# Kernel tuning notes

Measured on AMD Instinct MI355X. Metric: run time of the kernel, lower is better.

The kernel has to match this reference:

```python
import jax, jax.numpy as jnp
import numpy as np

B, P = 4, 50000
D_IN, COND = 3, 48
# layer l: in IN_DIMS[l] -> out OUT_DIMS[l]; dims=[3,256*8,257], skip at layer index 4
IN_DIMS  = [D_IN + COND, 256, 256, 256, 256, 256, 256, 256, 256]
OUT_DIMS = [256, 256, 256, 253, 256, 256, 256, 256, 257]
N_LIN = 9
INV_SQRT2 = np.float32(1.0 / np.sqrt(2.0))


def softplus_beta100(x):
    return jax.nn.softplus(100.0 * x) * 0.01


def setup_inputs() -> dict:
    key = jax.random.key(0)
    ks = jax.random.split(key, 2 + 2 * N_LIN)
    inp = {
        "input": jax.random.normal(ks[0], (B, P, D_IN), dtype=jnp.float32),
        "cond_pose": jax.random.normal(ks[1], (B, COND), dtype=jnp.float32),
    }
    for l in range(N_LIN):
        scale = np.float32(np.sqrt(2.0 / OUT_DIMS[l]))  # geometry-style init scale
        inp[f"W{l}"] = jax.random.normal(ks[2 + 2 * l], (OUT_DIMS[l], IN_DIMS[l]), dtype=jnp.float32) * scale
        inp[f"b{l}"] = jnp.zeros((OUT_DIMS[l],), dtype=jnp.float32)
    return inp


def reference(input, cond_pose,
              W0, b0, W1, b1, W2, b2, W3, b3, W4, b4, W5, b5, W6, b6, W7, b7, W8, b8):
    Ws = [W0, W1, W2, W3, W4, W5, W6, W7, W8]
    bs = [b0, b1, b2, b3, b4, b5, b6, b7, b8]
    nb, npnt, nd = input.shape
    x_in = input.reshape(nb * npnt, nd)                                   # (N, 3)
    c = jnp.broadcast_to(cond_pose[:, None, :], (nb, npnt, COND)).reshape(nb * npnt, COND)
    x = jnp.concatenate([x_in, c], axis=-1)                               # cond concat at layer 0
    for l in range(N_LIN):
        if l == 4:  # skip connection: concat raw input, scaled by 1/sqrt(2)
            x = jnp.concatenate([x, x_in], axis=-1) * INV_SQRT2
        x = x @ Ws[l].T + bs[l]
        if l < N_LIN - 1:
            x = softplus_beta100(x)
    return x.reshape(nb, npnt, -1)                                        # (B, P, 257)
```

## Files before the change

### kernel.cpp

```cpp
#include <hip/hip_runtime.h>


typedef __attribute__((ext_vector_type(8))) short bf16x8;
typedef __attribute__((ext_vector_type(4))) float f32x4;
typedef __attribute__((ext_vector_type(2))) float f32x2;

#define PPTS 50000

__device__ __forceinline__ short f2bf(float f) {
    union { float f; unsigned u; } v; v.f = f;
    unsigned r = v.u + 0x7fffu + ((v.u >> 16) & 1u);
    return (short)(r >> 16);
}

__device__ __forceinline__ unsigned cvt_pk_bf16(float lo, float hi) {
    unsigned r;
    asm("v_cvt_pk_bf16_f32 %0, %1, %2" : "=v"(r) : "v"(lo), "v"(hi));
    return r;
}

__device__ __forceinline__ f32x2 sp100_pair(f32x2 y) {
    const f32x2 A2 = {6.9314718e-3f, 6.9314718e-3f};
    const f32x2 B2 = {-3.11522e-3f, -3.11522e-3f};
    const f32x2 C2 = {9.8829e-4f,  9.8829e-4f};
    const f32x2 K2 = {-144.26950408889634f, -144.26950408889634f};
    const f32x2 Z2 = {0.0f, 0.0f};
    f32x2 m = __builtin_elementwise_abs(y) * K2;
    f32x2 e = {__builtin_amdgcn_exp2f(m.x), __builtin_amdgcn_exp2f(m.y)};
    f32x2 t = __builtin_elementwise_fma(C2, e, B2);
    t = __builtin_elementwise_fma(t, e, A2);
    return __builtin_elementwise_fma(e, t, __builtin_elementwise_max(y, Z2));
}

__device__ __forceinline__ int xswz(int row) {
    return (((row & 7) ^ (5 * ((row >> 3) & 1))) << 4);
}
__device__ __forceinline__ short* xaddr(short* base, int row, int col) {
    int off = ((row << 9) + (col << 1)) ^ xswz(row);
    return (short*)((char*)base + off);
}
__device__ __forceinline__ const short* xaddrc(const short* base, int row, int col) {
    int off = ((row << 9) + (col << 1)) ^ xswz(row);
    return (const short*)((const char*)base + off);
}

__global__ void prep_kernel(
    const float* __restrict__ W0, const float* __restrict__ W1, const float* __restrict__ W2,
    const float* __restrict__ W3, const float* __restrict__ W4, const float* __restrict__ W5,
    const float* __restrict__ W6, const float* __restrict__ W7, const float* __restrict__ W8,
    short* __restrict__ wbf)
{
    const int gid = blockIdx.x * blockDim.x + threadIdx.x;
    if (gid >= 68096) return;
    int l, cid; const float* Wsrc;
    if      (gid <  2048) { l = 0; cid = gid;         Wsrc = W0; }
    else if (gid < 10240) { l = 1; cid = gid -  2048; Wsrc = W1; }
    else if (gid < 18432) { l = 2; cid = gid - 10240; Wsrc = W2; }
    else if (gid < 26624) { l = 3; cid = gid - 18432; Wsrc = W3; }
    else if (gid < 34816) { l = 4; cid = gid - 26624; Wsrc = W4; }
    else if (gid < 43008) { l = 5; cid = gid - 34816; Wsrc = W5; }
    else if (gid < 51200) { l = 6; cid = gid - 43008; Wsrc = W6; }
    else if (gid < 59392) { l = 7; cid = gid - 51200; Wsrc = W7; }
    else                  { l = 8; cid = gid - 59392; Wsrc = W8; }
    const int NR   = (l == 3) ? 253 : ((l == 8) ? 257 : 256);
    const int KR   = (l == 0) ? 51 : 256;
    const int klog = (l == 0) ? 1 : 3;
    const float sc = (l == 4) ? 0.70710678f : 1.0f;
    const int lane  = cid & 63;
    const int tile  = cid >> 6;
    const int ntile = tile >> klog;
    const int ktile = tile & ((1 << klog) - 1);
    const int n  = ntile * 16 + (lane & 15);
    const int k0 = ktile * 32 + ((lane >> 4) << 3);
    bf16x8 v;
#pragma unroll
    for (int j = 0; j < 8; ++j) {
        int k = k0 + j;
        float f = (n < NR && k < KR) ? Wsrc[n * KR + k] * sc : 0.0f;
        v[j] = f2bf(f);
    }
    ((bf16x8*)wbf)[gid] = v;
}

template<int KSTEPS, int MODE>
__device__ __forceinline__ void layer_fwd(short* xb,
    const bf16x8* __restrict__ wl, const float* __restrict__ bias, int lane, int wid)
{
    const int prow = lane & 15;
    const int kg   = (lane >> 4) << 3;
    const int rb4  = (lane >> 4) << 2;
    f32x4 acc[4][4];
#pragma unroll
    for (int nii = 0; nii < 4; ++nii) {
        const int cb = (wid * 4 + nii) * 16 + rb4;
        f32x4 bv;
        if (MODE == 1 && cb == 252) { f32x4 tb = {bias[252], 0.f, 0.f, 0.f}; bv = tb; }
        else bv = *(const f32x4*)(bias + cb);
#pragma unroll
        for (int mi = 0; mi < 4; ++mi)
            acc[mi][nii] = bv;
    }
#pragma unroll 2
    for (int ks = 0; ks < KSTEPS; ++ks) {
        bf16x8 a[4], b[4];
#pragma unroll
        for (int nii = 0; nii < 4; ++nii)
            a[nii] = wl[((wid * 4 + nii) * KSTEPS + ks) * 64 + lane];
#pragma unroll
        for (int mi = 0; mi < 4; ++mi)
            b[mi] = *(const bf16x8*)xaddrc(xb, mi * 16 + prow, ks * 32 + kg);
#pragma unroll
        for (int mi = 0; mi < 4; ++mi)
#pragma unroll
            for (int nii = 0; nii < 4; ++nii)
                acc[mi][nii] = __builtin_amdgcn_mfma_f32_16x16x32_bf16(
                    a[nii], b[mi], acc[mi][nii], 0, 0, 0);
    }
#pragma unroll
    for (int nii = 0; nii < 4; ++nii)
#pragma unroll
        for (int mi = 0; mi < 4; ++mi) {
            f32x2 y0 = {acc[mi][nii][0], acc[mi][nii][1]};
            f32x2 y1 = {acc[mi][nii][2], acc[mi][nii][3]};
            f32x2 r0 = sp100_pair(y0);
            f32x2 r1 = sp100_pair(y1);
            acc[mi][nii][0] = r0.x; acc[mi][nii][1] = r0.y;
            acc[mi][nii][2] = r1.x; acc[mi][nii][3] = r1.y;
        }
    __syncthreads();
#pragma unroll
    for (int nii = 0; nii < 4; ++nii) {
        const int cb = (wid * 4 + nii) * 16 + rb4;
#pragma unroll
        for (int mi = 0; mi < 4; ++mi) {
            unsigned p01 = cvt_pk_bf16(acc[mi][nii][0], acc[mi][nii][1]);
            unsigned p23 = cvt_pk_bf16(acc[mi][nii][2], acc[mi][nii][3]);
            if (MODE == 1 && cb == 252) {
                *xaddr(xb, mi * 16 + prow, 252) = (short)(p01 & 0xffff);
            } else {
                uint2 pk; pk.x = p01; pk.y = p23;
                *(uint2*)xaddr(xb, mi * 16 + prow, cb) = pk;
            }
        }
    }
}

__global__ __launch_bounds__(256, 4) void net_kernel(
    const float* __restrict__ xin, const float* __restrict__ cond,
    const bf16x8* __restrict__ W,
    const float* __restrict__ b0, const float* __restrict__ b1, const float* __restrict__ b2,
    const float* __restrict__ b3, const float* __restrict__ b4, const float* __restrict__ b5,
    const float* __restrict__ b6, const float* __restrict__ b7, const float* __restrict__ b8,
    float* __restrict__ out)
{
    __shared__ short xb[64 * 256];
    const int t    = threadIdx.x;
    const int pt0  = blockIdx.x * 64;
    const int lane = t & 63;
    const int wid  = t >> 6;

    float sk[3] = {0.f, 0.f, 0.f};
    if (t < 64) {
#pragma unroll
        for (int c = 0; c < 3; ++c)
            sk[c] = xin[(pt0 + t) * 3 + c];
    }

    {
        const int row   = t >> 2;
        const int c0    = (t & 3) << 4;
        const int point = pt0 + row;
        const int batch = point / PPTS;
        const float* xp = xin + point * 3;
        const float* cp = cond + batch * 48;
#pragma unroll
        for (int h = 0; h < 2; ++h) {
            bf16x8 v;
#pragma unroll
            for (int i = 0; i < 8; ++i) {
                int c = c0 + h * 8 + i;
                float f = (c < 3) ? xp[c] : ((c < 51) ? cp[c - 3] : 0.0f);
                v[i] = f2bf(f);
            }
            *(bf16x8*)xaddr(xb, row, c0 + h * 8) = v;
        }
    }
    __syncthreads();

    layer_fwd<2, 0>(xb, W +     0, b0, lane, wid); __syncthreads();
    layer_fwd<8, 0>(xb, W +  2048, b1, lane, wid); __syncthreads();
    layer_fwd<8, 0>(xb, W + 10240, b2, lane, wid); __syncthreads();
    layer_fwd<8, 1>(xb, W + 18432, b3, lane, wid);
    if (t < 64) {
#pragma unroll
        for (int c = 0; c < 3; ++c)
            *xaddr(xb, t, 253 + c) = f2bf(sk[c]);
    }
    __syncthreads();
    layer_fwd<8, 0>(xb, W + 26624, b4, lane, wid); __syncthreads();
    layer_fwd<8, 0>(xb, W + 34816, b5, lane, wid); __syncthreads();
    layer_fwd<8, 0>(xb, W + 43008, b6, lane, wid); __syncthreads();
    layer_fwd<8, 0>(xb, W + 51200, b7, lane, wid); __syncthreads();

    {
        const bf16x8* wl = W + 59392;
        const int prow = lane & 15;
        const int kg   = (lane >> 4) << 3;
        const int rb4  = (lane >> 4) << 2;
        const float blast = b8[256];
#pragma unroll
        for (int half = 0; half < 2; ++half) {
            f32x4 acc[2][4];
            f32x4 acc2[2];
#pragma unroll
            for (int nii = 0; nii < 4; ++nii) {
                const int cb = (wid * 4 + nii) * 16 + rb4;
                const f32x4 bv = *(const f32x4*)(b8 + cb);
#pragma unroll
                for (int m2 = 0; m2 < 2; ++m2)
                    acc[m2][nii] = bv;
            }
            {
                f32x4 bz = {(rb4 == 0) ? blast : 0.f, 0.f, 0.f, 0.f};
                acc2[0] = bz; acc2[1] = bz;
            }
#pragma unroll 2
            for (int ks = 0; ks < 8; ++ks) {
                bf16x8 a[4], b[2], a2;
#pragma unroll
                for (int nii = 0; nii < 4; ++nii)
                    a[nii] = wl[((wid * 4 + nii) * 8 + ks) * 64 + lane];
                if (wid == 0) a2 = wl[(128 + ks) * 64 + lane];
#pragma unroll
                for (int m2 = 0; m2 < 2; ++m2)
                    b[m2] = *(const bf16x8*)xaddrc(xb, (half * 2 + m2) * 16 + prow,
                                                   ks * 32 + kg);
#pragma unroll
                for (int m2 = 0; m2 < 2; ++m2)
#pragma unroll
                    for (int nii = 0; nii < 4; ++nii)
                        acc[m2][nii] = __builtin_amdgcn_mfma_f32_16x16x32_bf16(
                            a[nii], b[m2], acc[m2][nii], 0, 0, 0);
                if (wid == 0) {
#pragma unroll
                    for (int m2 = 0; m2 < 2; ++m2)
                        acc2[m2] = __builtin_amdgcn_mfma_f32_16x16x32_bf16(
                            a2, b[m2], acc2[m2], 0, 0, 0);
                }
            }
#pragma unroll
            for (int nii = 0; nii < 4; ++nii) {
                const int cb = (wid * 4 + nii) * 16 + rb4;
#pragma unroll
                for (int m2 = 0; m2 < 2; ++m2) {
                    const int rowoff = (pt0 + (half * 2 + m2) * 16 + prow) * 257 + cb;
#pragma unroll
                    for (int r = 0; r < 4; ++r)
                        out[rowoff + r] = acc[m2][nii][r];
                }
            }
            if (wid == 0 && rb4 == 0) {
#pragma unroll
                for (int m2 = 0; m2 < 2; ++m2)
                    out[(pt0 + (half * 2 + m2) * 16 + prow) * 257 + 256]
                        = acc2[m2][0];
            }
        }
    }
}

extern "C" void kernel_launch(void* const* d_in, const int* in_sizes, int n_in,
                              void* d_out, int out_size, void* d_ws, size_t ws_size,
                              hipStream_t stream)
{
    const float* xin  = (const float*)d_in[0];
    const float* cond = (const float*)d_in[1];
    const float* Wp[9]; const float* bp[9];
    for (int l = 0; l < 9; ++l) { Wp[l] = (const float*)d_in[2 + 2 * l]; bp[l] = (const float*)d_in[3 + 2 * l]; }
    short* wbf = (short*)d_ws;

    prep_kernel<<<dim3(266), dim3(256), 0, stream>>>(
        Wp[0], Wp[1], Wp[2], Wp[3], Wp[4], Wp[5], Wp[6], Wp[7], Wp[8], wbf);
    net_kernel<<<dim3(3125), dim3(256), 0, stream>>>(
        xin, cond, (const bf16x8*)wbf,
        bp[0], bp[1], bp[2], bp[3], bp[4], bp[5], bp[6], bp[7], bp[8],
        (float*)d_out);
}
```

Baseline: 319.1 us.

## Prefetch next layer's first weight fragments during softplus epilogue and use lightweight barriers

Each layer now issues the global loads for the next layer's first k-step weight fragments before running the softplus epilogue, so the latency of the first weight load at each layer start is hidden. Block barriers become a custom sequence that waits only on LDS counters, letting outstanding global prefetches stay in flight across the barrier. Launch bounds drop from 4 to 3 blocks per SM to give room for the extra live registers, at the cost of lower occupancy.

```diff
diff --git a/kernel.cpp b/kernel.cpp
--- a/kernel.cpp
+++ b/kernel.cpp
@@ -17,6 +17,12 @@
     unsigned r;
     asm("v_cvt_pk_bf16_f32 %0, %1, %2" : "=v"(r) : "v"(lo), "v"(hi));
     return r;
+}
+
+__device__ __forceinline__ void bar_lgkm() {
+    asm volatile("s_waitcnt lgkmcnt(0)" ::: "memory");
+    __builtin_amdgcn_s_barrier();
+    __builtin_amdgcn_sched_barrier(0);
 }
 
 __device__ __forceinline__ f32x2 sp100_pair(f32x2 y) {
@@ -84,7 +90,8 @@
 
 template<int KSTEPS, int MODE>
 __device__ __forceinline__ void layer_fwd(short* xb,
-    const bf16x8* __restrict__ wl, const float* __restrict__ bias, int lane, int wid)
+    const bf16x8* __restrict__ wl, const bf16x8* __restrict__ wlnext,
+    const float* __restrict__ bias, int lane, int wid, bf16x8 (&apre)[4])
 {
     const int prow = lane & 15;
     const int kg   = (lane >> 4) << 3;
@@ -105,7 +112,8 @@
         bf16x8 a[4], b[4];
 #pragma unroll
         for (int nii = 0; nii < 4; ++nii)
-            a[nii] = wl[((wid * 4 + nii) * KSTEPS + ks) * 64 + lane];
+            a[nii] = (ks == 0) ? apre[nii]
+                               : wl[((wid * 4 + nii) * KSTEPS + ks) * 64 + lane];
 #pragma unroll
         for (int mi = 0; mi < 4; ++mi)
             b[mi] = *(const bf16x8*)xaddrc(xb, mi * 16 + prow, ks * 32 + kg);
@@ -116,6 +124,9 @@
                 acc[mi][nii] = __builtin_amdgcn_mfma_f32_16x16x32_bf16(
                     a[nii], b[mi], acc[mi][nii], 0, 0, 0);
     }
+#pragma unroll
+    for (int nii = 0; nii < 4; ++nii)
+        apre[nii] = wlnext[(wid * 4 + nii) * 512 + lane];
 #pragma unroll
     for (int nii = 0; nii < 4; ++nii)
 #pragma unroll
@@ -127,7 +138,7 @@
             acc[mi][nii][0] = r0.x; acc[mi][nii][1] = r0.y;
             acc[mi][nii][2] = r1.x; acc[mi][nii][3] = r1.y;
         }
-    __syncthreads();
+    bar_lgkm();
 #pragma unroll
     for (int nii = 0; nii < 4; ++nii) {
         const int cb = (wid * 4 + nii) * 16 + rb4;
@@ -145,7 +156,7 @@
     }
 }
 
-__global__ __launch_bounds__(256, 4) void net_kernel(
+__global__ __launch_bounds__(256, 3) void net_kernel(
     const float* __restrict__ xin, const float* __restrict__ cond,
     const bf16x8* __restrict__ W,
     const float* __restrict__ b0, const float* __restrict__ b1, const float* __restrict__ b2,
@@ -159,6 +170,11 @@
     const int lane = t & 63;
     const int wid  = t >> 6;
 
+    bf16x8 apre[4];
+#pragma unroll
+    for (int nii = 0; nii < 4; ++nii)
+        apre[nii] = W[(wid * 4 + nii) * 128 + lane];
+
     float sk[3] = {0.f, 0.f, 0.f};
     if (t < 64) {
 #pragma unroll
@@ -185,22 +201,22 @@
             *(bf16x8*)xaddr(xb, row, c0 + h * 8) = v;
         }
     }
-    __syncthreads();
-
-    layer_fwd<2, 0>(xb, W +     0, b0, lane, wid); __syncthreads();
-    layer_fwd<8, 0>(xb, W +  2048, b1, lane, wid); __syncthreads();
-    layer_fwd<8, 0>(xb, W + 10240, b2, lane, wid); __syncthreads();
-    layer_fwd<8, 1>(xb, W + 18432, b3, lane, wid);
+    bar_lgkm();
+
+    layer_fwd<2, 0>(xb, W +     0, W +  2048, b0, lane, wid, apre); bar_lgkm();
+    layer_fwd<8, 0>(xb, W +  2048, W + 10240, b1, lane, wid, apre); bar_lgkm();
+    layer_fwd<8, 0>(xb, W + 10240, W + 18432, b2, lane, wid, apre); bar_lgkm();
+    layer_fwd<8, 1>(xb, W + 18432, W + 26624, b3, lane, wid, apre);
     if (t < 64) {
 #pragma unroll
         for (int c = 0; c < 3; ++c)
             *xaddr(xb, t, 253 + c) = f2bf(sk[c]);
     }
-    __syncthreads();
-    layer_fwd<8, 0>(xb, W + 26624, b4, lane, wid); __syncthreads();
-    layer_fwd<8, 0>(xb, W + 34816, b5, lane, wid); __syncthreads();
-    layer_fwd<8, 0>(xb, W + 43008, b6, lane, wid); __syncthreads();
-    layer_fwd<8, 0>(xb, W + 51200, b7, lane, wid); __syncthreads();
+    bar_lgkm();
+    layer_fwd<8, 0>(xb, W + 26624, W + 34816, b4, lane, wid, apre); bar_lgkm();
+    layer_fwd<8, 0>(xb, W + 34816, W + 43008, b5, lane, wid, apre); bar_lgkm();
+    layer_fwd<8, 0>(xb, W + 43008, W + 51200, b6, lane, wid, apre); bar_lgkm();
+    layer_fwd<8, 0>(xb, W + 51200, W + 59392, b7, lane, wid, apre); bar_lgkm();
 
     {
         const bf16x8* wl = W + 59392;
@@ -229,7 +245,8 @@
                 bf16x8 a[4], b[2], a2;
 #pragma unroll
                 for (int nii = 0; nii < 4; ++nii)
-                    a[nii] = wl[((wid * 4 + nii) * 8 + ks) * 64 + lane];
+                    a[nii] = (half == 0 && ks == 0) ? apre[nii]
+                             : wl[((wid * 4 + nii) * 8 + ks) * 64 + lane];
                 if (wid == 0) a2 = wl[(128 + ks) * 64 + lane];
 #pragma unroll
                 for (int m2 = 0; m2 < 2; ++m2)
```

Result: faster. 303.0 us (-5.1%).
